# Kernel tuning notes

Measured on AMD Instinct MI355X. Metric: run time of the kernel, lower is better.

The kernel has to match this reference:

```python
import jax, jax.numpy as jnp
import numpy as np

N_HEADS = 16
ROPE_BASE = 10000.0

def apply_rope(x):
    # x: [B, H, S, D] with D even; interleaved-pair RoPE (torchtune style)
    B, H, S, D = x.shape
    half = D // 2
    inv_freq = 1.0 / (ROPE_BASE ** (jnp.arange(0, half, dtype=jnp.float32) / half))
    angles = jnp.arange(S, dtype=jnp.float32)[:, None] * inv_freq[None, :]  # [S, D/2]
    cos = jnp.cos(angles)[None, None]  # [1,1,S,D/2]
    sin = jnp.sin(angles)[None, None]
    x1 = x[..., 0::2]
    x2 = x[..., 1::2]
    r1 = x1 * cos - x2 * sin
    r2 = x1 * sin + x2 * cos
    return jnp.stack([r1, r2], axis=-1).reshape(B, H, S, D)

def setup_inputs() -> dict:
    key = jax.random.key(0)
    ks = jax.random.split(key, 5)
    B, S, E = 2, 2048, 1024
    d_attn = 1024
    scale = 1.0 / np.sqrt(E)
    x = jax.random.normal(ks[0], (B, S, E), dtype=jnp.float32)
    Wq = jax.random.normal(ks[1], (d_attn, E), dtype=jnp.float32) * scale
    Wk = jax.random.normal(ks[2], (d_attn, E), dtype=jnp.float32) * scale
    Wv = jax.random.normal(ks[3], (d_attn, E), dtype=jnp.float32) * scale
    Wo = jax.random.normal(ks[4], (E, d_attn), dtype=jnp.float32) * scale
    return {"x": x, "Wq": Wq, "Wk": Wk, "Wv": Wv, "Wo": Wo}

def reference(x, Wq, Wk, Wv, Wo):
    B, S, E = x.shape
    d_attn = Wq.shape[0]
    hd = d_attn // N_HEADS
    attn_scale = 1.0 / np.sqrt(d_attn)
    # projections (nn.Linear: x @ W.T), split heads -> [B, H, S, hd]
    q = (x @ Wq.T).reshape(B, S, N_HEADS, hd).transpose(0, 2, 1, 3)
    k = (x @ Wk.T).reshape(B, S, N_HEADS, hd).transpose(0, 2, 1, 3)
    v = (x @ Wv.T).reshape(B, S, N_HEADS, hd).transpose(0, 2, 1, 3)
    q = apply_rope(q)
    k = apply_rope(k)
    scores = jnp.einsum('bhqd,bhkd->bhqk', q, k) * attn_scale  # [B,H,S,S]
    causal = jnp.tril(jnp.ones((S, S), dtype=bool))
    scores = jnp.where(causal[None, None], scores, -jnp.inf)
    probs = jax.nn.softmax(scores, axis=-1)  # dropout is identity in eval
    out = jnp.einsum('bhqk,bhkd->bhqd', probs, v)
    out = out.transpose(0, 2, 1, 3).reshape(B, S, d_attn)
    return out @ Wo.T
```

## Files before the change

### kernel.cpp

```cpp
#include <hip/hip_runtime.h>


typedef float  f32x4  __attribute__((ext_vector_type(4)));
typedef short  short8 __attribute__((ext_vector_type(8)));

#define MFMA16(a,b,c) __builtin_amdgcn_mfma_f32_16x16x32_bf16((a),(b),(c),0,0,0)
#define GLD_LDS16(g, l)                                                        \
  __builtin_amdgcn_global_load_lds(                                            \
      (const __attribute__((address_space(1))) unsigned int*)(g),              \
      (__attribute__((address_space(3))) unsigned int*)(l), 16, 0, 0)

__device__ __forceinline__ unsigned short f2bf(float f) {
  unsigned int x = __float_as_uint(f);
  x += 0x7fffu + ((x >> 16) & 1u);
  return (unsigned short)(x >> 16);
}
__device__ __forceinline__ float bf2f(unsigned short u) {
  return __uint_as_float(((unsigned int)u) << 16);
}
__device__ __forceinline__ unsigned int cvtpk_bf16(float lo, float hi) {
  unsigned int r;
  asm("v_cvt_pk_bf16_f32 %0, %1, %2" : "=v"(r) : "v"(lo), "v"(hi));
  return r;
}

__global__ __launch_bounds__(256) void cvt_all(const float* __restrict__ x,
                                               const float* __restrict__ wq,
                                               const float* __restrict__ wk,
                                               const float* __restrict__ wv,
                                               const float* __restrict__ wo,
                                               ushort* __restrict__ dst) {
  const int i = blockIdx.x * 256 + threadIdx.x;
  const float* src;
  int off;
  if (i < 1048576) { src = x; off = i; }
  else {
    const int j = i - 1048576;
    const int wsel = j >> 18;
    off = j & 262143;
    src = (wsel == 0) ? wq : (wsel == 1) ? wk : (wsel == 2) ? wv : wo;
  }
  const float4 v = ((const float4*)src)[off];
  ushort4 o = make_ushort4(f2bf(v.x), f2bf(v.y), f2bf(v.z), f2bf(v.w));
  ((ushort4*)dst)[i] = o;
}

template<int MODE, int BN, int BM>
__global__ __launch_bounds__(256) void gemm_bt(const ushort* __restrict__ A,
                                               const ushort* __restrict__ B,
                                               void* __restrict__ Cv,
                                               int K) {
  constexpr int NI = BN / 32;
  constexpr int MI = BM / 32;
  constexpr int AI = BM / 64;
  constexpr int BI = BN / 64;
  __shared__ __align__(16) short As0[BM * 32];
  __shared__ __align__(16) short As1[BM * 32];
  __shared__ __align__(16) short Bs0[BN * 32];
  __shared__ __align__(16) short Bs1[BN * 32];
  const int tid  = threadIdx.x;
  const int lane = tid & 63, w = tid >> 6;
  const int ln   = lane & 15, quad = lane >> 4;
  const int wm   = w >> 1, wn = w & 1;
  const int m0 = blockIdx.y * BM, n0 = blockIdx.x * BN;

  const int srow = lane >> 2;
  const int schk = (lane & 3) * 8;
  const int arow = w * (16 * AI);
  const int brow = w * (16 * BI);
  const ushort* Ag0 = A + (size_t)(m0 + arow + srow) * K + schk;
  const ushort* Ag1 = A + (size_t)(m0 + arow + 16 + srow) * K + schk;
  const ushort* Bg0 = B + (size_t)(n0 + brow + srow) * K + schk;
  const ushort* Bg1 = B + (size_t)(n0 + brow + 16 + srow) * K + schk;
  const int lA0 = arow * 32, lA1 = (arow + 16) * 32;
  const int lB0 = brow * 32, lB1 = (brow + 16) * 32;

  int aoff[MI], boff[NI];
#pragma unroll
  for (int i = 0; i < MI; i++)
    aoff[i] = (wm * (BM / 2) + i * 16 + ln) * 32 + quad * 8;
#pragma unroll
  for (int i = 0; i < NI; i++)
    boff[i] = (wn * (BN / 2) + i * 16 + ln) * 32 + quad * 8;
  f32x4 acc[MI][NI] = {};

  for (int kt = 0; kt < K; kt += 64) {
    __syncthreads();
    GLD_LDS16(Ag0 + kt, As0 + lA0);
    if (AI == 2) GLD_LDS16(Ag1 + kt, As0 + lA1);
    GLD_LDS16(Ag0 + kt + 32, As1 + lA0);
    if (AI == 2) GLD_LDS16(Ag1 + kt + 32, As1 + lA1);
    GLD_LDS16(Bg0 + kt, Bs0 + lB0);
    if (BI == 2) GLD_LDS16(Bg1 + kt, Bs0 + lB1);
    GLD_LDS16(Bg0 + kt + 32, Bs1 + lB0);
    if (BI == 2) GLD_LDS16(Bg1 + kt + 32, Bs1 + lB1);
    __syncthreads();
#pragma unroll
    for (int h = 0; h < 2; ++h) {
      const short* Ap = h ? As1 : As0;
      const short* Bp = h ? Bs1 : Bs0;
      short8 av[MI], bv[NI];
#pragma unroll
      for (int i = 0; i < MI; i++) av[i] = *(const short8*)&Ap[aoff[i]];
#pragma unroll
      for (int i = 0; i < NI; i++) bv[i] = *(const short8*)&Bp[boff[i]];
#pragma unroll
      for (int mi = 0; mi < MI; mi++)
#pragma unroll
        for (int ni = 0; ni < NI; ni++)
          acc[mi][ni] = MFMA16(av[mi], bv[ni], acc[mi][ni]);
    }
  }

  if (MODE == 0) {
    ushort* Cq = (ushort*)Cv;
    if (n0 < 2048) {
      ushort* dst = Cq + (n0 < 1024 ? 0 : 4194304);
      const int nbase = (n0 < 1024) ? n0 : n0 - 1024;
      const float qsc = (n0 < 1024) ? 0.04508422002778011f : 1.0f;
      const float sgn = (ln & 1) ? 1.0f : -1.0f;
      float invc[NI];
#pragma unroll
      for (int ni = 0; ni < NI; ni++) {
        const int ii = ((wn * (BN / 2) + ni * 16 + ln) & 63) >> 1;
        invc[ni] = __builtin_amdgcn_exp2f(-(float)ii * 0.4152410118579865f) *
                   0.15915494309189535f;
      }
#pragma unroll
      for (int mi = 0; mi < MI; mi++) {
        const int row = m0 + wm * (BM / 2) + mi * 16 + quad * 4;
#pragma unroll
        for (int ni = 0; ni < NI; ni++) {
          const int col = nbase + wn * (BN / 2) + ni * 16 + ln;
#pragma unroll
          for (int r = 0; r < 4; r++) {
            const float mine  = acc[mi][ni][r];
            const float other = __shfl_xor(mine, 1, 64);
            const int   s     = (row + r) & 2047;
            const float rev   = (float)s * invc[ni];
            const float rr    = rev - floorf(rev);
            const float sn = __builtin_amdgcn_sinf(rr);
            const float cs = __builtin_amdgcn_cosf(rr);
            const float rot = (mine * cs + sgn * other * sn) * qsc;
            dst[(size_t)(row + r) * 1024 + col] = f2bf(rot);
          }
        }
      }
    } else {
      ushort* vt = Cq + 8388608;
#pragma unroll
      for (int mi = 0; mi < MI; mi++) {
        const int sm = m0 + wm * (BM / 2) + mi * 16 + quad * 4;
        const int b = sm >> 11, s = sm & 2047;
#pragma unroll
        for (int ni = 0; ni < NI; ni++) {
          const int nv = (n0 - 2048) + wn * (BN / 2) + ni * 16 + ln;
          const int bh = b * 16 + (nv >> 6), d = nv & 63;
          ushort4 u = make_ushort4(f2bf(acc[mi][ni][0]), f2bf(acc[mi][ni][1]),
                                   f2bf(acc[mi][ni][2]), f2bf(acc[mi][ni][3]));
          *(ushort4*)&vt[((size_t)bh * 64 + d) * 2048 + s] = u;
        }
      }
    }
  } else {
    float* C = (float*)Cv;
#pragma unroll
    for (int mi = 0; mi < MI; mi++) {
      const int row = m0 + wm * (BM / 2) + mi * 16 + quad * 4;
#pragma unroll
      for (int ni = 0; ni < NI; ni++) {
        const int col = n0 + wn * (BN / 2) + ni * 16 + ln;
#pragma unroll
        for (int r = 0; r < 4; r++)
          C[(size_t)(row + r) * 1024 + col] = acc[mi][ni][r];
      }
    }
  }
}

__global__ __launch_bounds__(256) void attnk(const ushort* __restrict__ q,
                                             const ushort* __restrict__ k,
                                             const ushort* __restrict__ vt,
                                             ushort* __restrict__ ctx) {
  __shared__ __align__(16) short Ks[2][64 * 72];
  __shared__ __align__(16) short Vs[2][64 * 72];
  __shared__ __align__(16) short PsB[4 * 16 * 72];
  __shared__ __align__(16) short PsA[4 * 16 * 72];
  const int tid  = threadIdx.x;
  const int lane = tid & 63, w = tid >> 6;
  const int ln   = lane & 15, quad = lane >> 4;
  const int x = blockIdx.x, bh = blockIdx.y;
  const int b = bh >> 4, h = bh & 15;
  const int jA = x, jB = 31 - x;
  short* PwB = PsB + w * 1152;
  short* PwA = PsA + w * 1152;

  const size_t qbA = ((size_t)(b * 2048 + jA * 64 + w * 16 + ln)) * 1024 + h * 64;
  const size_t qbB = ((size_t)(b * 2048 + jB * 64 + w * 16 + ln)) * 1024 + h * 64;
  const short8 aqA0 = *(const short8*)&q[qbA + quad * 8];
  const short8 aqA1 = *(const short8*)&q[qbA + 32 + quad * 8];
  const short8 aqB0 = *(const short8*)&q[qbB + quad * 8];
  const short8 aqB1 = *(const short8*)&q[qbB + 32 + quad * 8];

  f32x4 oA[4] = {}, oB[4] = {};
  float lsA0 = 0.f, lsA1 = 0.f, lsB0 = 0.f, lsB1 = 0.f;

  const int s0 = tid, s1 = tid + 256;
  const int r0 = s0 >> 3, c0 = (s0 & 7) * 8;
  const int r1 = s1 >> 3, c1 = (s1 & 7) * 8;
  const ushort* kg0 = k  + ((size_t)(b * 2048 + r0)) * 1024 + h * 64 + c0;
  const ushort* kg1 = k  + ((size_t)(b * 2048 + r1)) * 1024 + h * 64 + c1;
  const ushort* vg0 = vt + ((size_t)(bh * 64 + r0)) * 2048 + c0;
  const ushort* vg1 = vt + ((size_t)(bh * 64 + r1)) * 2048 + c1;
  const int wK0 = r0 * 72 + c0, wK1 = r1 * 72 + c1;

  short8 kr0 = *(const short8*)(kg0);
  short8 kr1 = *(const short8*)(kg1);
  short8 vr0 = *(const short8*)(vg0);
  short8 vr1 = *(const short8*)(vg1);
  *(short8*)&Ks[0][wK0] = kr0;
  *(short8*)&Ks[0][wK1] = kr1;
  *(short8*)&Vs[0][wK0] = vr0;
  *(short8*)&Vs[0][wK1] = vr1;
  kr0 = *(const short8*)(kg0 + 65536);
  kr1 = *(const short8*)(kg1 + 65536);
  vr0 = *(const short8*)(vg0 + 64);
  vr1 = *(const short8*)(vg1 + 64);

  const int qlocB = jB * 64 + w * 16 + ln;
  const int qlocA = jA * 64 + w * 16 + ln;

  for (int t = 0; t <= jB; t++) {
    __syncthreads();
    const short* Kc = Ks[t & 1];
    const short* Vc = Vs[t & 1];
    if (t < jB) {
      short* Kn = (short*)Ks[(t & 1) ^ 1];
      short* Vn = (short*)Vs[(t & 1) ^ 1];
      *(short8*)&Kn[wK0] = kr0;
      *(short8*)&Kn[wK1] = kr1;
      *(short8*)&Vn[wK0] = vr0;
      *(short8*)&Vn[wK1] = vr1;
    }
    if (t + 2 <= jB) {
      kr0 = *(const short8*)(kg0 + (size_t)(t + 2) * 65536);
      kr1 = *(const short8*)(kg1 + (size_t)(t + 2) * 65536);
      vr0 = *(const short8*)(vg0 + (t + 2) * 64);
      vr1 = *(const short8*)(vg1 + (t + 2) * 64);
    }

    const bool actA = (t <= jA);
    f32x4 scA[4], scB[4];
#pragma unroll
    for (int ct = 0; ct < 4; ct++) {
      const short8 bk0 = *(const short8*)&Kc[(ct * 16 + ln) * 72 + quad * 8];
      const short8 bk1 = *(const short8*)&Kc[(ct * 16 + ln) * 72 + 32 + quad * 8];
      f32x4 z = {0.f, 0.f, 0.f, 0.f};
      z = MFMA16(bk0, aqB0, z);
      z = MFMA16(bk1, aqB1, z);
      scB[ct] = z;
      if (actA) {
        f32x4 y = {0.f, 0.f, 0.f, 0.f};
        y = MFMA16(bk0, aqA0, y);
        y = MFMA16(bk1, aqA1, y);
        scA[ct] = y;
      }
    }
    if (t == jB) {
#pragma unroll
      for (int ct = 0; ct < 4; ct++) {
        const int kvb = (t << 6) + ct * 16 + quad * 4;
#pragma unroll
        for (int r = 0; r < 4; r++)
          if (kvb + r > qlocB) scB[ct][r] = -100000.0f;
      }
    }
    if (actA && t == jA) {
#pragma unroll
      for (int ct = 0; ct < 4; ct++) {
        const int kvb = (t << 6) + ct * 16 + quad * 4;
#pragma unroll
        for (int r = 0; r < 4; r++)
          if (kvb + r > qlocA) scA[ct][r] = -100000.0f;
      }
    }

    short8 bv0[4], bv1[4];
#pragma unroll
    for (int dt = 0; dt < 4; dt++) {
      bv0[dt] = *(const short8*)&Vc[(dt * 16 + ln) * 72 + quad * 8];
      bv1[dt] = *(const short8*)&Vc[(dt * 16 + ln) * 72 + 32 + quad * 8];
    }

#pragma unroll
    for (int ct = 0; ct < 4; ct++) {
      const float p0 = __builtin_amdgcn_exp2f(scB[ct][0]);
      const float p1 = __builtin_amdgcn_exp2f(scB[ct][1]);
      const float p2 = __builtin_amdgcn_exp2f(scB[ct][2]);
      const float p3 = __builtin_amdgcn_exp2f(scB[ct][3]);
      lsB0 += p0 + p1;
      lsB1 += p2 + p3;
      const uint2 u = make_uint2(cvtpk_bf16(p0, p1), cvtpk_bf16(p2, p3));
      *(uint2*)&PwB[ln * 72 + ct * 16 + quad * 4] = u;
    }
    {
      const short8 ap0 = *(const short8*)&PwB[ln * 72 + quad * 8];
      const short8 ap1 = *(const short8*)&PwB[ln * 72 + 32 + quad * 8];
#pragma unroll
      for (int dt = 0; dt < 4; dt++) {
        oB[dt] = MFMA16(ap0, bv0[dt], oB[dt]);
        oB[dt] = MFMA16(ap1, bv1[dt], oB[dt]);
      }
    }
    if (actA) {
#pragma unroll
      for (int ct = 0; ct < 4; ct++) {
        const float p0 = __builtin_amdgcn_exp2f(scA[ct][0]);
        const float p1 = __builtin_amdgcn_exp2f(scA[ct][1]);
        const float p2 = __builtin_amdgcn_exp2f(scA[ct][2]);
        const float p3 = __builtin_amdgcn_exp2f(scA[ct][3]);
        lsA0 += p0 + p1;
        lsA1 += p2 + p3;
        const uint2 u = make_uint2(cvtpk_bf16(p0, p1), cvtpk_bf16(p2, p3));
        *(uint2*)&PwA[ln * 72 + ct * 16 + quad * 4] = u;
      }
      const short8 ap0 = *(const short8*)&PwA[ln * 72 + quad * 8];
      const short8 ap1 = *(const short8*)&PwA[ln * 72 + 32 + quad * 8];
#pragma unroll
      for (int dt = 0; dt < 4; dt++) {
        oA[dt] = MFMA16(ap0, bv0[dt], oA[dt]);
        oA[dt] = MFMA16(ap1, bv1[dt], oA[dt]);
      }
    }
  }

  float lA = lsA0 + lsA1, lB = lsB0 + lsB1;
  lA += __shfl_xor(lA, 16, 64);
  lA += __shfl_xor(lA, 32, 64);
  lB += __shfl_xor(lB, 16, 64);
  lB += __shfl_xor(lB, 32, 64);

#pragma unroll
  for (int r = 0; r < 4; r++) {
    const float invA = 1.0f / __shfl(lA, quad * 4 + r, 64);
    const float invB = 1.0f / __shfl(lB, quad * 4 + r, 64);
    const int rowA = jA * 64 + w * 16 + quad * 4 + r;
    const int rowB = jB * 64 + w * 16 + quad * 4 + r;
#pragma unroll
    for (int dt = 0; dt < 4; dt++) {
      ctx[((size_t)(b * 2048 + rowA)) * 1024 + h * 64 + dt * 16 + ln] =
          f2bf(oA[dt][r] * invA);
      ctx[((size_t)(b * 2048 + rowB)) * 1024 + h * 64 + dt * 16 + ln] =
          f2bf(oB[dt][r] * invB);
    }
  }
}

extern "C" void kernel_launch(void* const* d_in, const int* in_sizes, int n_in,
                              void* d_out, int out_size, void* d_ws, size_t ws_size,
                              hipStream_t stream) {
  const float* x  = (const float*)d_in[0];
  const float* Wq = (const float*)d_in[1];
  const float* Wk = (const float*)d_in[2];
  const float* Wv = (const float*)d_in[3];
  const float* Wo = (const float*)d_in[4];
  float* out = (float*)d_out;
  char* ws = (char*)d_ws;

  ushort* xb  = (ushort*)(ws);
  ushort* wqb = (ushort*)(ws + (size_t)(8  << 20));
  ushort* qb  = (ushort*)(ws + (size_t)(16 << 20));
  ushort* kb  = (ushort*)(ws + (size_t)(24 << 20));
  ushort* vtb = (ushort*)(ws + (size_t)(32 << 20));
  ushort* ctx = (ushort*)(ws + (size_t)(40 << 20));

  cvt_all<<<8192, 256, 0, stream>>>(x, Wq, Wk, Wv, Wo, xb);
  gemm_bt<0, 64, 128><<<dim3(48, 32), 256, 0, stream>>>(xb, wqb, (void*)qb, 1024);
  attnk<<<dim3(16, 32), 256, 0, stream>>>(qb, kb, vtb, ctx);
  gemm_bt<2, 64, 64><<<dim3(16, 64), 256, 0, stream>>>(ctx, wqb + 3145728 , (void*)out, 1024);
}
```

Before: 180.4 us.

## Double-buffer GEMM K-loop so global-to-LDS loads overlap MFMA compute

Restructures the bf16 GEMM main loop into a ping-pong pipeline over two 32-wide K slices. The next slice is issued with global_load_lds while MFMAs consume the current one, instead of loading both halves and then computing behind a barrier. This targets memory latency that was exposed in the projection and output GEMMs. Barrier count per iteration stays the same, but correctness relies on __syncthreads draining the asynchronous LDS loads.

```diff
diff --git a/kernel.cpp b/kernel.cpp
--- a/kernel.cpp
+++ b/kernel.cpp
@@ -54,10 +54,8 @@
   constexpr int MI = BM / 32;
   constexpr int AI = BM / 64;
   constexpr int BI = BN / 64;
-  __shared__ __align__(16) short As0[BM * 32];
-  __shared__ __align__(16) short As1[BM * 32];
-  __shared__ __align__(16) short Bs0[BN * 32];
-  __shared__ __align__(16) short Bs1[BN * 32];
+  __shared__ __align__(16) short As[2][BM * 32];
+  __shared__ __align__(16) short Bs[2][BN * 32];
   const int tid  = threadIdx.x;
   const int lane = tid & 63, w = tid >> 6;
   const int ln   = lane & 15, quad = lane >> 4;
@@ -84,32 +82,34 @@
     boff[i] = (wn * (BN / 2) + i * 16 + ln) * 32 + quad * 8;
   f32x4 acc[MI][NI] = {};
 
+  auto stage = [&](short* Ad, short* Bd, int kt) {
+    GLD_LDS16(Ag0 + kt, Ad + lA0);
+    if (AI == 2) GLD_LDS16(Ag1 + kt, Ad + lA1);
+    GLD_LDS16(Bg0 + kt, Bd + lB0);
+    if (BI == 2) GLD_LDS16(Bg1 + kt, Bd + lB1);
+  };
+  auto compute = [&](const short* Ap, const short* Bp) {
+    short8 av[MI], bv[NI];
+#pragma unroll
+    for (int i = 0; i < MI; i++) av[i] = *(const short8*)&Ap[aoff[i]];
+#pragma unroll
+    for (int i = 0; i < NI; i++) bv[i] = *(const short8*)&Bp[boff[i]];
+#pragma unroll
+    for (int mi = 0; mi < MI; mi++)
+#pragma unroll
+      for (int ni = 0; ni < NI; ni++)
+        acc[mi][ni] = MFMA16(av[mi], bv[ni], acc[mi][ni]);
+  };
+
+  stage(As[0], Bs[0], 0);
+  __syncthreads();
   for (int kt = 0; kt < K; kt += 64) {
+    if (kt + 32 < K) stage(As[1], Bs[1], kt + 32);
+    compute(As[0], Bs[0]);
     __syncthreads();
-    GLD_LDS16(Ag0 + kt, As0 + lA0);
-    if (AI == 2) GLD_LDS16(Ag1 + kt, As0 + lA1);
-    GLD_LDS16(Ag0 + kt + 32, As1 + lA0);
-    if (AI == 2) GLD_LDS16(Ag1 + kt + 32, As1 + lA1);
-    GLD_LDS16(Bg0 + kt, Bs0 + lB0);
-    if (BI == 2) GLD_LDS16(Bg1 + kt, Bs0 + lB1);
-    GLD_LDS16(Bg0 + kt + 32, Bs1 + lB0);
-    if (BI == 2) GLD_LDS16(Bg1 + kt + 32, Bs1 + lB1);
+    if (kt + 64 < K) stage(As[0], Bs[0], kt + 64);
+    compute(As[1], Bs[1]);
     __syncthreads();
-#pragma unroll
-    for (int h = 0; h < 2; ++h) {
-      const short* Ap = h ? As1 : As0;
-      const short* Bp = h ? Bs1 : Bs0;
-      short8 av[MI], bv[NI];
-#pragma unroll
-      for (int i = 0; i < MI; i++) av[i] = *(const short8*)&Ap[aoff[i]];
-#pragma unroll
-      for (int i = 0; i < NI; i++) bv[i] = *(const short8*)&Bp[boff[i]];
-#pragma unroll
-      for (int mi = 0; mi < MI; mi++)
-#pragma unroll
-        for (int ni = 0; ni < NI; ni++)
-          acc[mi][ni] = MFMA16(av[mi], bv[ni], acc[mi][ni]);
-    }
   }
 
   if (MODE == 0) {
```

After: 191.1 us. +5.9%, slower.
